# Optimization experiments

Measured on AMD Instinct MI355X. Metric: run time of the kernel, lower is better.

The kernel has to match this reference:

```python
import jax, jax.numpy as jnp
import numpy as np

V = 16384  # points per mesh


def _nn_idx(q, r):
    """1-NN index into r for each row of q. q: [Vq,3], r: [Vr,3] -> [Vq] int32.

    Squared euclidean distance via ||q||^2 - 2 q.r + ||r||^2 (K=1 knn_points).
    """
    d = (jnp.sum(q * q, axis=-1, keepdims=True)
         - 2.0 * (q @ r.T)
         + jnp.sum(r * r, axis=-1)[None, :])  # [Vq, Vr]
    return jnp.argmin(d, axis=1)


def setup_inputs() -> dict:
    key = jax.random.key(0)
    k1, k2, k3, k4 = jax.random.split(key, 4)
    return {
        "pred_vertices": jax.random.normal(k1, (1, V, 3), dtype=jnp.float32),
        "trg_vertices": jax.random.normal(k2, (1, V, 3), dtype=jnp.float32),
        "pred_e": jax.random.normal(k3, (1, V, 3), dtype=jnp.float32),
        "trg_e": jax.random.normal(k4, (1, V, 3), dtype=jnp.float32),
    }


def reference(pred_vertices, trg_vertices, pred_e, trg_e):
    pv = pred_vertices[0]  # [V,3]
    tv = trg_vertices[0]   # [V,3]
    # knn_points runs under torch.no_grad() -> indices are constants
    trg2pred_idx = jax.lax.stop_gradient(_nn_idx(tv, pv))  # [V]
    pred2trg_idx = jax.lax.stop_gradient(_nn_idx(pv, tv))  # [V]
    loss_trg2pred = jnp.mean((trg_e - pred_e[:, trg2pred_idx, :]) ** 2)
    loss_pred2trg = jnp.mean((pred_e - trg_e[:, pred2trg_idx, :]) ** 2)
    return loss_trg2pred + loss_pred2trg
```

## Files before the change

kernel.cpp:

```cpp
#include <hip/hip_runtime.h>
#include <hip/hip_bf16.h>

#define NV 16384
#define NT 256
#define NTILES 512
#define RT_CHUNK 64
#define NCHUNK (NTILES / RT_CHUNK)
#define STG 32
#define RES_QPB 4
#define RES_BLOCKS (NV / RES_QPB)
#define NPART (2 * RES_BLOCKS)

typedef __attribute__((ext_vector_type(8))) short bf16x8;
typedef __attribute__((ext_vector_type(16))) float f32x16;

__device__ __forceinline__ short bf16bits(float f) {
    __hip_bfloat16 h = __float2bfloat16(f);
    return *reinterpret_cast<short*>(&h);
}
__device__ __forceinline__ float bf16tof(short s) {
    __hip_bfloat16 h = *reinterpret_cast<__hip_bfloat16*>(&s);
    return __bfloat162float(h);
}
__device__ __forceinline__ unsigned sortable(float f) {
    unsigned u = __float_as_uint(f);
    return (u & 0x80000000u) ? ~u : (u | 0x80000000u);
}
__device__ __forceinline__ float min3f(float a, float b, float c) {
    float r;
    asm("v_min3_f32 %0, %1, %2, %3" : "=v"(r) : "v"(a), "v"(b), "v"(c));
    return r;
}
__device__ __forceinline__ float tree16(const f32x16& c) {
    float t0 = min3f(c[0], c[1], c[2]);
    float t1 = min3f(c[3], c[4], c[5]);
    float t2 = min3f(c[6], c[7], c[8]);
    float t3 = min3f(c[9], c[10], c[11]);
    float t4 = min3f(c[12], c[13], c[14]);
    float s0 = min3f(t0, t1, c[15]);
    float s1 = min3f(t2, t3, t4);
    return fminf(s0, s1);
}

__device__ __forceinline__ bf16x8 make_a(float x, float y, float z, int half) {
    short hx = bf16bits(x), hy = bf16bits(y), hz = bf16bits(z);
    short lx = bf16bits(x - bf16tof(hx));
    short ly = bf16bits(y - bf16tof(hy));
    short lz = bf16bits(z - bf16tof(hz));
    float n  = 0.5f * fmaf(z, z, fmaf(y, y, x * x));
    short nh = bf16bits(n);
    short nl = bf16bits(n - bf16tof(nh));
    bf16x8 v;
    v[0] = half ? hz : hx;  v[1] = half ? nh : hy;
    v[2] = half ? nl : hz;  v[3] = half ? (short)0 : lx;
    v[4] = half ? (short)0 : ly;  v[5] = half ? (short)0 : lz;
    v[6] = half ? (short)0 : hx;  v[7] = half ? (short)0 : hy;
    return v;
}
__device__ __forceinline__ bf16x8 make_b(float x, float y, float z, int half) {
    short hx = bf16bits(x), hy = bf16bits(y), hz = bf16bits(z);
    short nhx = bf16bits(-x), nhy = bf16bits(-y), nhz = bf16bits(-z);
    short nlx = bf16bits(bf16tof(hx) - x);
    short nly = bf16bits(bf16tof(hy) - y);
    short nlz = bf16bits(bf16tof(hz) - z);
    const short one = 0x3F80;
    bf16x8 v;
    v[0] = half ? nlz : nhx;  v[1] = half ? one : nhy;
    v[2] = half ? one : nhz;  v[3] = half ? (short)0 : nhx;
    v[4] = half ? (short)0 : nhy;  v[5] = half ? (short)0 : nhz;
    v[6] = half ? (short)0 : nlx;  v[7] = half ? (short)0 : nly;
    return v;
}

__global__ __launch_bounds__(NT, 4) void nn_mfma_kernel(
    const float* __restrict__ pred_v, const float* __restrict__ trg_v,
    unsigned long long* __restrict__ results)
{
    __shared__ short lds[STG * 512];
    const int tid = threadIdx.x, lane = tid & 63, w = tid >> 6;
    const int dir = blockIdx.z;
    const float* qpts = dir ? pred_v : trg_v;
    const float* rpts = dir ? trg_v : pred_v;
    const int qt0 = blockIdx.x * 8 + w * 2;
    const int rtb = blockIdx.y * RT_CHUNK;
    const int half = lane >> 5;

    const int qp0 = qt0 * 32 + (lane & 31);
    bf16x8 b0 = make_b(qpts[3 * qp0 + 0], qpts[3 * qp0 + 1], qpts[3 * qp0 + 2], half);
    bf16x8 b1 = make_b(qpts[3 * (qp0 + 32) + 0], qpts[3 * (qp0 + 32) + 1],
                       qpts[3 * (qp0 + 32) + 2], half);

    float dmin0 = 1e30f, dmin1 = 1e30f;
    int bp0 = 0, bp1 = 0;
    const f32x16 zc = {};

    for (int g = 0; g < RT_CHUNK / STG; g++) {
        __syncthreads();
        for (int s = tid; s < STG * 64; s += NT) {
            int t = s >> 6, l = s & 63;
            int rp = (rtb + g * STG + t) * 32 + (l & 31);
            bf16x8 va = make_a(rpts[3 * rp + 0], rpts[3 * rp + 1], rpts[3 * rp + 2], l >> 5);
            *(bf16x8*)(&lds[t * 512 + l * 8]) = va;
        }
        __syncthreads();
#pragma unroll 2
        for (int p = 0; p < STG / 2; p++) {
            bf16x8 a0 = *(const bf16x8*)(&lds[(2 * p) * 512 + lane * 8]);
            f32x16 c0 = __builtin_amdgcn_mfma_f32_32x32x16_bf16(a0, b0, zc, 0, 0, 0);
            f32x16 c1 = __builtin_amdgcn_mfma_f32_32x32x16_bf16(a0, b1, zc, 0, 0, 0);
            float u0 = tree16(c0), u1 = tree16(c1);
            bf16x8 a1 = *(const bf16x8*)(&lds[(2 * p + 1) * 512 + lane * 8]);
            f32x16 d0 = __builtin_amdgcn_mfma_f32_32x32x16_bf16(a1, b0, zc, 0, 0, 0);
            f32x16 d1 = __builtin_amdgcn_mfma_f32_32x32x16_bf16(a1, b1, zc, 0, 0, 0);
            float m0 = fminf(u0, tree16(d0));
            float m1 = fminf(u1, tree16(d1));
            int pid = blockIdx.y * (RT_CHUNK / 2) + g * (STG / 2) + p;
            bool lt0 = m0 < dmin0; dmin0 = lt0 ? m0 : dmin0; bp0 = lt0 ? pid : bp0;
            bool lt1 = m1 < dmin1; dmin1 = lt1 ? m1 : dmin1; bp1 = lt1 ? pid : bp1;
        }
    }

    unsigned long long k0 = ((unsigned long long)sortable(dmin0) << 32) | (unsigned)bp0;
    unsigned long long k1 = ((unsigned long long)sortable(dmin1) << 32) | (unsigned)bp1;
    unsigned long long o0 = __shfl_xor(k0, 32); k0 = (o0 < k0) ? o0 : k0;
    unsigned long long o1 = __shfl_xor(k1, 32); k1 = (o1 < k1) ? o1 : k1;
    if (lane < 32) {
        size_t base = ((size_t)dir * NCHUNK + blockIdx.y) * NV;
        results[base + qt0 * 32 + lane] = k0;
        results[base + (qt0 + 1) * 32 + lane] = k1;
    }
}

__global__ __launch_bounds__(NT) void resolve_loss_kernel(
    const float* __restrict__ pred_v, const float* __restrict__ trg_v,
    const float* __restrict__ pred_e, const float* __restrict__ trg_e,
    const unsigned long long* __restrict__ results, float* __restrict__ partials)
{
    const int dir = blockIdx.y;
    const float* qpts = dir ? pred_v : trg_v;
    const float* rpts = dir ? trg_v : pred_v;
    const float* qe_b = dir ? pred_e : trg_e;
    const float* re_b = dir ? trg_e : pred_e;

    const int tid = threadIdx.x, lane = tid & 63, wv = tid >> 6;
    const int q = blockIdx.x * RES_QPB + wv;

    unsigned long long key = 0xFFFFFFFFFFFFFFFFULL;
    if (lane < NCHUNK)
        key = results[((size_t)dir * NCHUNK + lane) * NV + q];
    unsigned long long o;
    o = __shfl_xor(key, 4); key = (o < key) ? o : key;
    o = __shfl_xor(key, 2); key = (o < key) ? o : key;
    o = __shfl_xor(key, 1); key = (o < key) ? o : key;
    key = __shfl(key, 0);
    const int pair = (int)(unsigned)(key & 0xFFFFFFFFULL);
    const int i = pair * 64 + lane;

    float nqx = -qpts[3 * q + 0], nqy = -qpts[3 * q + 1], nqz = -qpts[3 * q + 2];
    float x = rpts[3 * i + 0], y = rpts[3 * i + 1], z = rpts[3 * i + 2];
    float rw = 0.5f * fmaf(z, z, fmaf(y, y, x * x));
    float s = fmaf(nqx, x, rw);
    s = fmaf(nqy, y, s);
    s = fmaf(nqz, z, s);

    unsigned long long kk = ((unsigned long long)sortable(s) << 32) | (unsigned)i;
#pragma unroll
    for (int off = 32; off > 0; off >>= 1) {
        unsigned long long t = __shfl_xor(kk, off);
        kk = (t < kk) ? t : kk;
    }

    __shared__ float wsum[RES_QPB];
    if (lane == 0) {
        int j = (int)(unsigned)(kk & 0xFFFFFFFFULL);
        float dx = qe_b[3 * q + 0] - re_b[3 * j + 0];
        float dy = qe_b[3 * q + 1] - re_b[3 * j + 1];
        float dz = qe_b[3 * q + 2] - re_b[3 * j + 2];
        wsum[wv] = fmaf(dx, dx, fmaf(dy, dy, dz * dz));
    }
    __syncthreads();
    if (tid == 0)
        partials[dir * RES_BLOCKS + blockIdx.x] =
            (wsum[0] + wsum[1]) + (wsum[2] + wsum[3]);
}

__global__ __launch_bounds__(NT) void final_kernel(
    const float* __restrict__ partials, float* __restrict__ out)
{
    const int tid = threadIdx.x;
    float acc = 0.0f;
#pragma unroll
    for (int t = 0; t < NPART / NT; t++) acc += partials[t * NT + tid];
    __shared__ float red[NT];
    red[tid] = acc;
    __syncthreads();
    for (int s = NT / 2; s > 0; s >>= 1) {
        if (tid < s) red[tid] += red[tid + s];
        __syncthreads();
    }
    if (tid == 0) out[0] = red[0] * (1.0f / 49152.0f);
}

extern "C" void kernel_launch(void* const* d_in, const int* in_sizes, int n_in,
                              void* d_out, int out_size, void* d_ws, size_t ws_size,
                              hipStream_t stream) {
    const float* pred_v = (const float*)d_in[0];
    const float* trg_v  = (const float*)d_in[1];
    const float* pred_e = (const float*)d_in[2];
    const float* trg_e  = (const float*)d_in[3];
    float* out = (float*)d_out;

    unsigned long long* results = (unsigned long long*)d_ws;
    float* partials = (float*)(results + 2 * NCHUNK * NV);

    nn_mfma_kernel<<<dim3(NTILES / 8, NCHUNK, 2), NT, 0, stream>>>(pred_v, trg_v, results);

    resolve_loss_kernel<<<dim3(RES_BLOCKS, 2), NT, 0, stream>>>(
        pred_v, trg_v, pred_e, trg_e, results, partials);

    final_kernel<<<1, NT, 0, stream>>>(partials, out);
}
```

Measured before the change: 39.06 us.

## Precompute packed bf16 reference operands once and batch resolve queries per wave

Adds a prep kernel that builds the split-bf16 MFMA A-operand fragments for all reference points once and writes them to workspace. The NN kernel then copies these packed fragments straight into LDS instead of recomputing them in every block, which removes redundant conversion work repeated across the 64 query-tile blocks. The resolve kernel now handles 4 queries per wave, so it launches a quarter as many blocks and writes fewer partials. In exchange there is an extra kernel launch and more global memory traffic for the packed buffer.

Result: no change. 39.48 us (+1.1%).

```diff
diff --git a/kernel.cpp b/kernel.cpp
--- a/kernel.cpp
+++ b/kernel.cpp
@@ -7,7 +7,10 @@
 #define RT_CHUNK 64
 #define NCHUNK (NTILES / RT_CHUNK)
 #define STG 32
-#define RES_QPB 4
+#define QT_PER_BLOCK 8
+#define NN_BX (NTILES / QT_PER_BLOCK)
+#define RES_QPW 4
+#define RES_QPB (4 * RES_QPW)
 #define RES_BLOCKS (NV / RES_QPB)
 #define NPART (2 * RES_BLOCKS)
 
@@ -72,18 +75,33 @@
     return v;
 }
 
+__global__ __launch_bounds__(NT) void prep_kernel(
+    const float* __restrict__ pred_v, const float* __restrict__ trg_v,
+    short* __restrict__ Apack)
+{
+    int gid = blockIdx.x * NT + threadIdx.x;
+    int d   = gid >> 15;
+    int rem = gid & 32767;
+    int t   = rem >> 6;
+    int l   = rem & 63;
+    const float* rpts = d ? trg_v : pred_v;
+    int p = t * 32 + (l & 31);
+    bf16x8 v = make_a(rpts[3 * p + 0], rpts[3 * p + 1], rpts[3 * p + 2], l >> 5);
+    *(bf16x8*)(Apack + ((size_t)gid) * 8) = v;
+}
+
 __global__ __launch_bounds__(NT, 4) void nn_mfma_kernel(
     const float* __restrict__ pred_v, const float* __restrict__ trg_v,
-    unsigned long long* __restrict__ results)
+    const short* __restrict__ Apack, unsigned long long* __restrict__ results)
 {
     __shared__ short lds[STG * 512];
     const int tid = threadIdx.x, lane = tid & 63, w = tid >> 6;
     const int dir = blockIdx.z;
     const float* qpts = dir ? pred_v : trg_v;
-    const float* rpts = dir ? trg_v : pred_v;
-    const int qt0 = blockIdx.x * 8 + w * 2;
+    const int qt0 = blockIdx.x * QT_PER_BLOCK + w * 2;
     const int rtb = blockIdx.y * RT_CHUNK;
     const int half = lane >> 5;
+    const size_t dbase = (size_t)dir * NTILES * 512;
 
     const int qp0 = qt0 * 32 + (lane & 31);
     bf16x8 b0 = make_b(qpts[3 * qp0 + 0], qpts[3 * qp0 + 1], qpts[3 * qp0 + 2], half);
@@ -96,11 +114,11 @@
 
     for (int g = 0; g < RT_CHUNK / STG; g++) {
         __syncthreads();
-        for (int s = tid; s < STG * 64; s += NT) {
-            int t = s >> 6, l = s & 63;
-            int rp = (rtb + g * STG + t) * 32 + (l & 31);
-            bf16x8 va = make_a(rpts[3 * rp + 0], rpts[3 * rp + 1], rpts[3 * rp + 2], l >> 5);
-            *(bf16x8*)(&lds[t * 512 + l * 8]) = va;
+        const bf16x8* src = (const bf16x8*)(Apack + dbase + (size_t)(rtb + g * STG) * 512);
+#pragma unroll
+        for (int s = 0; s < (STG * 64) / NT; s++) {
+            int slot = s * NT + tid;
+            *(bf16x8*)(&lds[slot * 8]) = src[slot];
         }
         __syncthreads();
 #pragma unroll 2
@@ -143,41 +161,46 @@
     const float* re_b = dir ? trg_e : pred_e;
 
     const int tid = threadIdx.x, lane = tid & 63, wv = tid >> 6;
-    const int q = blockIdx.x * RES_QPB + wv;
-
-    unsigned long long key = 0xFFFFFFFFFFFFFFFFULL;
-    if (lane < NCHUNK)
-        key = results[((size_t)dir * NCHUNK + lane) * NV + q];
-    unsigned long long o;
-    o = __shfl_xor(key, 4); key = (o < key) ? o : key;
-    o = __shfl_xor(key, 2); key = (o < key) ? o : key;
-    o = __shfl_xor(key, 1); key = (o < key) ? o : key;
-    key = __shfl(key, 0);
-    const int pair = (int)(unsigned)(key & 0xFFFFFFFFULL);
-    const int i = pair * 64 + lane;
-
-    float nqx = -qpts[3 * q + 0], nqy = -qpts[3 * q + 1], nqz = -qpts[3 * q + 2];
-    float x = rpts[3 * i + 0], y = rpts[3 * i + 1], z = rpts[3 * i + 2];
-    float rw = 0.5f * fmaf(z, z, fmaf(y, y, x * x));
-    float s = fmaf(nqx, x, rw);
-    s = fmaf(nqy, y, s);
-    s = fmaf(nqz, z, s);
-
-    unsigned long long kk = ((unsigned long long)sortable(s) << 32) | (unsigned)i;
+    float acc = 0.0f;
+
+    for (int qq = 0; qq < RES_QPW; qq++) {
+        const int q = blockIdx.x * RES_QPB + wv * RES_QPW + qq;
+
+        unsigned long long key = 0xFFFFFFFFFFFFFFFFULL;
+        if (lane < NCHUNK)
+            key = results[((size_t)dir * NCHUNK + lane) * NV + q];
+        unsigned long long o;
+        o = __shfl_xor(key, 4); key = (o < key) ? o : key;
+        o = __shfl_xor(key, 2); key = (o < key) ? o : key;
+        o = __shfl_xor(key, 1); key = (o < key) ? o : key;
+        key = __shfl(key, 0);
+        const int pair = (int)(unsigned)(key & 0xFFFFFFFFULL);
+        const int i = pair * 64 + lane;
+
+        float nqx = -qpts[3 * q + 0], nqy = -qpts[3 * q + 1], nqz = -qpts[3 * q + 2];
+        float x = rpts[3 * i + 0], y = rpts[3 * i + 1], z = rpts[3 * i + 2];
+        float rw = 0.5f * fmaf(z, z, fmaf(y, y, x * x));
+        float s = fmaf(nqx, x, rw);
+        s = fmaf(nqy, y, s);
+        s = fmaf(nqz, z, s);
+
+        unsigned long long kk = ((unsigned long long)sortable(s) << 32) | (unsigned)i;
 #pragma unroll
-    for (int off = 32; off > 0; off >>= 1) {
-        unsigned long long t = __shfl_xor(kk, off);
-        kk = (t < kk) ? t : kk;
-    }
-
-    __shared__ float wsum[RES_QPB];
-    if (lane == 0) {
-        int j = (int)(unsigned)(kk & 0xFFFFFFFFULL);
-        float dx = qe_b[3 * q + 0] - re_b[3 * j + 0];
-        float dy = qe_b[3 * q + 1] - re_b[3 * j + 1];
-        float dz = qe_b[3 * q + 2] - re_b[3 * j + 2];
-        wsum[wv] = fmaf(dx, dx, fmaf(dy, dy, dz * dz));
-    }
+        for (int off = 32; off > 0; off >>= 1) {
+            unsigned long long t = __shfl_xor(kk, off);
+            kk = (t < kk) ? t : kk;
+        }
+        if (lane == 0) {
+            int j = (int)(unsigned)(kk & 0xFFFFFFFFULL);
+            float dx = qe_b[3 * q + 0] - re_b[3 * j + 0];
+            float dy = qe_b[3 * q + 1] - re_b[3 * j + 1];
+            float dz = qe_b[3 * q + 2] - re_b[3 * j + 2];
+            acc += fmaf(dx, dx, fmaf(dy, dy, dz * dz));
+        }
+    }
+
+    __shared__ float wsum[4];
+    if (lane == 0) wsum[wv] = acc;
     __syncthreads();
     if (tid == 0)
         partials[dir * RES_BLOCKS + blockIdx.x] =
@@ -211,9 +234,13 @@
     float* out = (float*)d_out;
 
     unsigned long long* results = (unsigned long long*)d_ws;
-    float* partials = (float*)(results + 2 * NCHUNK * NV);
-
-    nn_mfma_kernel<<<dim3(NTILES / 8, NCHUNK, 2), NT, 0, stream>>>(pred_v, trg_v, results);
+    short* Apack = (short*)(results + 2 * NCHUNK * NV);
+    float* partials = (float*)(Apack + 2 * NTILES * 512);
+
+    prep_kernel<<<(2 * NTILES * 64) / NT, NT, 0, stream>>>(pred_v, trg_v, Apack);
+
+    nn_mfma_kernel<<<dim3(NN_BX, NCHUNK, 2), NT, 0, stream>>>(
+        pred_v, trg_v, Apack, results);
 
     resolve_loss_kernel<<<dim3(RES_BLOCKS, 2), NT, 0, stream>>>(
         pred_v, trg_v, pred_e, trg_e, results, partials);
```
